# Performance work log

Measured on AMD Instinct MI355X. Metric: run time of the kernel, lower is better.

Reference implementation:

```python
import jax, jax.numpy as jnp
import numpy as np

IN_FEATURES = 128
OUT_FEATURES = 128
N_HEADS = 64
BATCH = 8192


def setup_inputs() -> dict:
    key = jax.random.key(0)
    k_x, k_h, k_w = jax.random.split(key, 3)
    x = jax.random.normal(k_x, (BATCH, IN_FEATURES), dtype=jnp.float32)
    head_ix = jax.random.randint(k_h, (BATCH,), 0, N_HEADS, dtype=jnp.int64)
    stdv = 1.0 / np.sqrt(OUT_FEATURES)
    weight = jax.random.uniform(
        k_w, (N_HEADS, IN_FEATURES, OUT_FEATURES), dtype=jnp.float32,
        minval=-stdv, maxval=stdv)
    bias = jnp.zeros((N_HEADS, OUT_FEATURES), dtype=jnp.float32)
    return {"input": x, "weight": weight, "bias": bias, "head_ix": head_ix}


def reference(input, weight, bias, head_ix):
    # Gather per-row weight matrix [B, in, out] and bias [B, out], then
    # batched vector-matrix multiply: einsum('ab,abc->ac').
    w = weight[head_ix]            # [B, in, out]
    b = bias[head_ix]              # [B, out]
    out = jnp.einsum('bi,bio->bo', input, w) + b
    return out
```

## Files before the change

### kernel.cpp

```cpp
#include <hip/hip_runtime.h>

#define NHEADS 64
#define INF    128
#define OUTF   128
#define SPLITS 8
#define BLOCK  256

__global__ __launch_bounds__(BLOCK) void fused_headgemv(
    const float* __restrict__ x, const float* __restrict__ W,
    const float* __restrict__ bias, const int* __restrict__ hix,
    float* __restrict__ out, int n) {
  __shared__ float Ws[INF * OUTF];

  const int h    = blockIdx.x;
  const int s    = blockIdx.y;
  const int tid  = threadIdx.x;
  const int lane = tid & 63;
  const int w    = tid >> 6;

  {
    const float4* Wg = (const float4*)(W + (size_t)h * (INF * OUTF));
    float4* Wl = (float4*)Ws;
#pragma unroll
    for (int t = 0; t < (INF * OUTF / 4) / BLOCK; ++t)
      Wl[tid + t * BLOCK] = Wg[tid + t * BLOCK];
  }
  __syncthreads();

  const float b0 = bias[h * OUTF + lane];
  const float b1 = bias[h * OUTF + 64 + lane];

  const int range = n / SPLITS;
  const int sub   = s * range + w * (range / 4);
  unsigned long long mask[4];
#pragma unroll
  for (int c = 0; c < 4; ++c) {
    int r  = sub + c * 64 + lane;
    int hv = (r < n) ? hix[r] : -1;
    mask[c] = __ballot(hv == h);
  }

  int c = 0;
  unsigned long long m = mask[0];
  for (;;) {
    int rows[4];
    int nr = 0;
    while (nr < 4) {
      while (m == 0ull && c < 3) m = mask[++c];
      if (m == 0ull) break;
      int b = __ffsll((unsigned long long)m) - 1;
      m &= (m - 1);
      rows[nr++] = __builtin_amdgcn_readfirstlane(sub + c * 64 + b);
    }
    if (nr == 0) break;
#pragma unroll
    for (int r = nr; r < 4; ++r) rows[r] = rows[0];

    const float* xr0 = x + (size_t)rows[0] * INF;
    const float* xr1 = x + (size_t)rows[1] * INF;
    const float* xr2 = x + (size_t)rows[2] * INF;
    const float* xr3 = x + (size_t)rows[3] * INF;

    float acc00 = b0, acc01 = b0, acc02 = b0, acc03 = b0;
    float acc10 = b1, acc11 = b1, acc12 = b1, acc13 = b1;

    for (int kc = 0; kc < INF / 8; ++kc) {
      float xs0[8], xs1[8], xs2[8], xs3[8];
#pragma unroll
      for (int i = 0; i < 8; ++i) {
        xs0[i] = xr0[kc * 8 + i];
        xs1[i] = xr1[kc * 8 + i];
        xs2[i] = xr2[kc * 8 + i];
        xs3[i] = xr3[kc * 8 + i];
      }
#pragma unroll
      for (int i = 0; i < 8; ++i) {
        const int k = kc * 8 + i;
        float w0 = Ws[k * OUTF + lane];
        float w1 = Ws[k * OUTF + 64 + lane];
        acc00 = fmaf(xs0[i], w0, acc00); acc10 = fmaf(xs0[i], w1, acc10);
        acc01 = fmaf(xs1[i], w0, acc01); acc11 = fmaf(xs1[i], w1, acc11);
        acc02 = fmaf(xs2[i], w0, acc02); acc12 = fmaf(xs2[i], w1, acc12);
        acc03 = fmaf(xs3[i], w0, acc03); acc13 = fmaf(xs3[i], w1, acc13);
      }
    }

    {
      float* o = out + (size_t)rows[0] * OUTF;
      o[lane] = acc00; o[64 + lane] = acc10;
    }
    if (nr > 1) {
      float* o = out + (size_t)rows[1] * OUTF;
      o[lane] = acc01; o[64 + lane] = acc11;
    }
    if (nr > 2) {
      float* o = out + (size_t)rows[2] * OUTF;
      o[lane] = acc02; o[64 + lane] = acc12;
    }
    if (nr > 3) {
      float* o = out + (size_t)rows[3] * OUTF;
      o[lane] = acc03; o[64 + lane] = acc13;
    }
  }
}

extern "C" void kernel_launch(void* const* d_in, const int* in_sizes, int n_in,
                              void* d_out, int out_size, void* d_ws, size_t ws_size,
                              hipStream_t stream) {
  const float* x    = (const float*)d_in[0];
  const float* W    = (const float*)d_in[1];
  const float* bias = (const float*)d_in[2];
  const int*   hix  = (const int*)d_in[3];
  float* out = (float*)d_out;

  const int n = in_sizes[3];

  dim3 grid(NHEADS, SPLITS);
  fused_headgemv<<<grid, BLOCK, 0, stream>>>(x, W, bias, hix, out, n);
}
```

Before: 81.62 us.

## Drop shared-memory weight staging, read weights from global, batch 8 rows

Removes the LDS copy of each head's 64KB weight matrix and the block barrier. Weights are now read as float2 straight from global memory, with each lane owning two adjacent output columns. Each wave processes up to 8 gathered rows at a time with float4 x loads, and the grid doubles to 16 splits. This cuts the upfront 64KB load and the occupancy limit that LDS imposed. The cost is that weight reads rely on L2/L1 cache hits and more blocks re-fetch the same weights.

```diff
diff --git a/kernel.cpp b/kernel.cpp
--- a/kernel.cpp
+++ b/kernel.cpp
@@ -3,104 +3,85 @@
 #define NHEADS 64
 #define INF    128
 #define OUTF   128
-#define SPLITS 8
+#define SPLITS 16
 #define BLOCK  256
+#define RROWS  8
+#define WMASKS 2
 
 __global__ __launch_bounds__(BLOCK) void fused_headgemv(
     const float* __restrict__ x, const float* __restrict__ W,
     const float* __restrict__ bias, const int* __restrict__ hix,
     float* __restrict__ out, int n) {
-  __shared__ float Ws[INF * OUTF];
-
   const int h    = blockIdx.x;
   const int s    = blockIdx.y;
-  const int tid  = threadIdx.x;
-  const int lane = tid & 63;
-  const int w    = tid >> 6;
-
-  {
-    const float4* Wg = (const float4*)(W + (size_t)h * (INF * OUTF));
-    float4* Wl = (float4*)Ws;
-#pragma unroll
-    for (int t = 0; t < (INF * OUTF / 4) / BLOCK; ++t)
-      Wl[tid + t * BLOCK] = Wg[tid + t * BLOCK];
-  }
-  __syncthreads();
-
-  const float b0 = bias[h * OUTF + lane];
-  const float b1 = bias[h * OUTF + 64 + lane];
+  const int lane = threadIdx.x & 63;
+  const int w    = threadIdx.x >> 6;
 
   const int range = n / SPLITS;
   const int sub   = s * range + w * (range / 4);
-  unsigned long long mask[4];
+
+  unsigned long long mask[WMASKS];
 #pragma unroll
-  for (int c = 0; c < 4; ++c) {
+  for (int c = 0; c < WMASKS; ++c) {
     int r  = sub + c * 64 + lane;
     int hv = (r < n) ? hix[r] : -1;
     mask[c] = __ballot(hv == h);
   }
 
+  const float2  bv = ((const float2*)(bias + (size_t)h * OUTF))[lane];
+  const float2* Wr = (const float2*)(W + (size_t)h * (INF * OUTF));
+
   int c = 0;
   unsigned long long m = mask[0];
   for (;;) {
-    int rows[4];
+    int rows[RROWS];
     int nr = 0;
-    while (nr < 4) {
-      while (m == 0ull && c < 3) m = mask[++c];
+    while (nr < RROWS) {
+      while (m == 0ull && c < WMASKS - 1) m = mask[++c];
       if (m == 0ull) break;
-      int b = __ffsll((unsigned long long)m) - 1;
-      m &= (m - 1);
+      int b = __ffsll(m) - 1;
+      m &= m - 1;
       rows[nr++] = __builtin_amdgcn_readfirstlane(sub + c * 64 + b);
     }
     if (nr == 0) break;
 #pragma unroll
-    for (int r = nr; r < 4; ++r) rows[r] = rows[0];
+    for (int r2 = 0; r2 < RROWS; ++r2)
+      if (r2 >= nr) rows[r2] = rows[0];
 
-    const float* xr0 = x + (size_t)rows[0] * INF;
-    const float* xr1 = x + (size_t)rows[1] * INF;
-    const float* xr2 = x + (size_t)rows[2] * INF;
-    const float* xr3 = x + (size_t)rows[3] * INF;
+    const float* xr[RROWS];
+#pragma unroll
+    for (int r2 = 0; r2 < RROWS; ++r2) xr[r2] = x + (size_t)rows[r2] * INF;
 
-    float acc00 = b0, acc01 = b0, acc02 = b0, acc03 = b0;
-    float acc10 = b1, acc11 = b1, acc12 = b1, acc13 = b1;
+    float2 acc[RROWS];
+#pragma unroll
+    for (int r2 = 0; r2 < RROWS; ++r2) acc[r2] = bv;
 
-    for (int kc = 0; kc < INF / 8; ++kc) {
-      float xs0[8], xs1[8], xs2[8], xs3[8];
+    for (int kc = 0; kc < INF; kc += 4) {
+      float4 xc[RROWS];
 #pragma unroll
-      for (int i = 0; i < 8; ++i) {
-        xs0[i] = xr0[kc * 8 + i];
-        xs1[i] = xr1[kc * 8 + i];
-        xs2[i] = xr2[kc * 8 + i];
-        xs3[i] = xr3[kc * 8 + i];
-      }
+      for (int r2 = 0; r2 < RROWS; ++r2)
+        xc[r2] = *(const float4*)(xr[r2] + kc);
+      float2 wv0 = Wr[(kc + 0) * 64 + lane];
+      float2 wv1 = Wr[(kc + 1) * 64 + lane];
+      float2 wv2 = Wr[(kc + 2) * 64 + lane];
+      float2 wv3 = Wr[(kc + 3) * 64 + lane];
 #pragma unroll
-      for (int i = 0; i < 8; ++i) {
-        const int k = kc * 8 + i;
-        float w0 = Ws[k * OUTF + lane];
-        float w1 = Ws[k * OUTF + 64 + lane];
-        acc00 = fmaf(xs0[i], w0, acc00); acc10 = fmaf(xs0[i], w1, acc10);
-        acc01 = fmaf(xs1[i], w0, acc01); acc11 = fmaf(xs1[i], w1, acc11);
-        acc02 = fmaf(xs2[i], w0, acc02); acc12 = fmaf(xs2[i], w1, acc12);
-        acc03 = fmaf(xs3[i], w0, acc03); acc13 = fmaf(xs3[i], w1, acc13);
+      for (int r2 = 0; r2 < RROWS; ++r2) {
+        acc[r2].x = fmaf(xc[r2].x, wv0.x, acc[r2].x);
+        acc[r2].y = fmaf(xc[r2].x, wv0.y, acc[r2].y);
+        acc[r2].x = fmaf(xc[r2].y, wv1.x, acc[r2].x);
+        acc[r2].y = fmaf(xc[r2].y, wv1.y, acc[r2].y);
+        acc[r2].x = fmaf(xc[r2].z, wv2.x, acc[r2].x);
+        acc[r2].y = fmaf(xc[r2].z, wv2.y, acc[r2].y);
+        acc[r2].x = fmaf(xc[r2].w, wv3.x, acc[r2].x);
+        acc[r2].y = fmaf(xc[r2].w, wv3.y, acc[r2].y);
       }
     }
 
-    {
-      float* o = out + (size_t)rows[0] * OUTF;
-      o[lane] = acc00; o[64 + lane] = acc10;
-    }
-    if (nr > 1) {
-      float* o = out + (size_t)rows[1] * OUTF;
-      o[lane] = acc01; o[64 + lane] = acc11;
-    }
-    if (nr > 2) {
-      float* o = out + (size_t)rows[2] * OUTF;
-      o[lane] = acc02; o[64 + lane] = acc12;
-    }
-    if (nr > 3) {
-      float* o = out + (size_t)rows[3] * OUTF;
-      o[lane] = acc03; o[64 + lane] = acc13;
-    }
+#pragma unroll
+    for (int r2 = 0; r2 < RROWS; ++r2)
+      if (r2 < nr)
+        ((float2*)(out + (size_t)rows[r2] * OUTF))[lane] = acc[r2];
   }
 }
 
```

Measured after the change: 87.27 us. 1.07x slower.
